# Kernel tuning notes

Measured on AMD Instinct MI355X. Metric: run time of the kernel, lower is better.

The kernel has to match this reference:

```python
import jax, jax.numpy as jnp
import numpy as np

NUM_EXPERTS = 8
HIDDEN = 2048
INTER = 4096
TOKENS = 8192  # divisible by NUM_EXPERTS


def setup_inputs() -> dict:
    key = jax.random.key(0)
    k1, k2, k3 = jax.random.split(key, 3)
    hidden_states = jax.random.normal(k1, (TOKENS, HIDDEN), dtype=jnp.float32)
    gate_up_proj = jax.random.normal(k2, (NUM_EXPERTS, HIDDEN, 2 * INTER), dtype=jnp.float32) * 0.02
    down_proj = jax.random.normal(k3, (NUM_EXPERTS, INTER, HIDDEN), dtype=jnp.float32) * 0.02
    return {"hidden_states": hidden_states, "gate_up_proj": gate_up_proj, "down_proj": down_proj}


def reference(hidden_states, gate_up_proj, down_proj):
    E, H = gate_up_proj.shape[0], gate_up_proj.shape[1]
    x = hidden_states.reshape(E, -1, H)                      # (E, T/E, H)
    gate_up = jnp.einsum('eth,ehf->etf', x, gate_up_proj)    # (E, T/E, 2I)
    gate, up = jnp.split(gate_up, 2, axis=-1)
    acted = up * jax.nn.silu(gate)                           # (E, T/E, I)
    out = jnp.einsum('eti,eih->eth', acted, down_proj)       # (E, T/E, H)
    return out.reshape(-1, H)
```

## Files before the change

kernel.cpp:

```cpp
#include <hip/hip_runtime.h>


#define E_   8
#define H_   2048
#define I_   4096
#define T_   8192
#define TPE  1024

typedef __bf16 bf16x8 __attribute__((ext_vector_type(8)));
typedef float  f32x4  __attribute__((ext_vector_type(4)));

__device__ __forceinline__ unsigned short f2bf(float f) {
  union { float f; unsigned int u; } v; v.f = f;
  unsigned int u = v.u;
  u += 0x7FFFu + ((u >> 16) & 1u);
  return (unsigned short)(u >> 16);
}

__device__ __forceinline__ void async16(const void* g, void* l) {
  __builtin_amdgcn_global_load_lds(
      (__attribute__((address_space(1))) void*)(g),
      (__attribute__((address_space(3))) void*)(l), 16, 0, 0);
}

#define SB0()    __builtin_amdgcn_sched_barrier(0)
#define BAR()    __builtin_amdgcn_s_barrier()
#define WAITLGKM() asm volatile("s_waitcnt lgkmcnt(0)" ::: "memory")
#define WAITVM(n)  asm volatile("s_waitcnt vmcnt(" #n ")" ::: "memory")

__global__ void convert_bf16(const float* __restrict__ src,
                             unsigned short* __restrict__ dst, long n) {
  long i = ((long)blockIdx.x * blockDim.x + threadIdx.x) * 4;
  const long stride = (long)gridDim.x * blockDim.x * 4;
  for (; i < n; i += stride) {
    const float4 v = *(const float4*)&src[i];
    ushort4 o;
    o.x = f2bf(v.x); o.y = f2bf(v.y); o.z = f2bf(v.z); o.w = f2bf(v.w);
    *(ushort4*)&dst[i] = o;
  }
}

template <int K, int NBN, int LDB, bool SILU>
__global__ __launch_bounds__(512, 2)
void gemm_fused(const unsigned short* __restrict__ Aall,
                const float* __restrict__ Ball,
                void* __restrict__ Cout,
                long sA, long sB, long sC) {
  extern __shared__ char smem[];
  constexpr int NT = K / 64;

  const int tid  = threadIdx.x;
  const int wave = tid >> 6;
  const int lane = tid & 63;
  const int lr   = lane & 15;
  const int lq   = lane >> 4;
  const int wid_m = wave >> 2;
  const int wid_n = wave & 3;

  const int nwg = gridDim.x;
  const int bid = blockIdx.x;
  const int wg  = (bid & 7) * (nwg >> 3) + (bid >> 3);
  const int mb  = wg & 3;
  const int tmp = wg >> 2;
  const int nb  = tmp % NBN;
  const int e   = tmp / NBN;

  const unsigned short* A = Aall + (long)e * sA + (long)(mb * 256) * K;
  const float*          B = Ball + (long)e * sB;

  const int stl  = tid >> 3;
  const int scol = ((tid & 7) ^ (stl & 7)) * 8;

  auto stageA = [&](int bi, int q, int kt) {
    const long col = (long)kt * 64 + scol;
    char* l0 = smem + bi * 32768 + q * 16384 + wave * 1024;
    async16(A + (long)(q * 64 + stl) * K + col,        l0);
    async16(A + (long)(128 + q * 64 + stl) * K + col,  l0 + 8192);
  };

  const int stB = tid & 255;
  int colg;
  {
    const int b  = stB >> 7;
    const int r  = stB & 127;
    const int w  = r >> 5;
    const int nf = (r >> 4) & 1;
    const int l4 = stB & 15;
    if (SILU) {
      const int c = w * 32 + b * 16 + l4;
      colg = nb * 128 + c + (nf ? I_ : 0);
    } else {
      colg = nb * 256 + w * 64 + (b * 2 + nf) * 16 + l4;
    }
  }
  const float* Bp = B + colg;
  const int koB = tid >> 8;

  float bv[16];
  auto loadB = [&](int g, int kt) {
#pragma unroll
    for (int uu = 0; uu < 2; ++uu) {
      const int ko = (g * 2 + uu) * 2 + koB;
      const long krow = (long)kt * 64 + ko * 8;
#pragma unroll
      for (int j = 0; j < 8; ++j)
        bv[uu * 8 + j] = Bp[(krow + j) * (long)LDB];
    }
  };
  auto writeB = [&](int bo, int g) {
    char* LB = smem + 65536 + bo * 32768;
#pragma unroll
    for (int uu = 0; uu < 2; ++uu) {
      const int ko = (g * 2 + uu) * 2 + koB;
      bf16x8 pk;
#pragma unroll
      for (int j = 0; j < 8; ++j) pk[j] = (__bf16)bv[uu * 8 + j];
      *(bf16x8*)(LB + stB * 128 + ((ko ^ (stB & 7)) * 16)) = pk;
    }
  };

  const int ax0 = ((0 + lq) ^ (lr & 7)) * 16;
  const int ax1 = ((4 + lq) ^ (lr & 7)) * 16;

  f32x4 acc[8][4];
#pragma unroll
  for (int m = 0; m < 8; ++m)
#pragma unroll
    for (int n = 0; n < 4; ++n) acc[m][n] = (f32x4)0.0f;

  const int t1p = (NT > 1) ? 1 : 0;
  loadB(0, 0);
  stageA(0, 0, 0);
  stageA(0, 1, 0);
  SB0();
  WAITVM(4);
  writeB(0, 0);
  loadB(1, 0);
  stageA(1, 0, t1p);
  stageA(1, 1, t1p);
  SB0();
  WAITVM(4);
  writeB(0, 1);
  WAITLGKM();
  BAR();

#pragma unroll 1
  for (int t = 0; t < NT; ++t) {
    const int cur = t & 1;
    const int bo  = cur ^ 1;
    const char* LA = smem + cur * 32768;
    const char* LB = smem + 65536 + cur * 32768;
    const int t1v = (t + 1 < NT) ? t + 1 : NT - 1;
    const int t2v = (t + 2 < NT) ? t + 2 : NT - 1;

    bf16x8 a[4][2], b0[2][2], b1[2][2];

#pragma unroll
    for (int mf = 0; mf < 4; ++mf) {
      const int st = wid_m * 64 + mf * 16 + lr;
      a[mf][0] = *(const bf16x8*)(LA + st * 128 + ax0);
      a[mf][1] = *(const bf16x8*)(LA + st * 128 + ax1);
    }
#pragma unroll
    for (int nf = 0; nf < 2; ++nf) {
      const int st = wid_n * 32 + nf * 16 + lr;
      b0[nf][0] = *(const bf16x8*)(LB + st * 128 + ax0);
      b0[nf][1] = *(const bf16x8*)(LB + st * 128 + ax1);
    }
    loadB(0, t1v);
    SB0();
    BAR();
    WAITLGKM();
    __builtin_amdgcn_s_setprio(1);
#pragma unroll
    for (int mf = 0; mf < 4; ++mf)
#pragma unroll
      for (int nf = 0; nf < 2; ++nf) {
        acc[mf][nf] = __builtin_amdgcn_mfma_f32_16x16x32_bf16(a[mf][0], b0[nf][0], acc[mf][nf], 0, 0, 0);
        acc[mf][nf] = __builtin_amdgcn_mfma_f32_16x16x32_bf16(a[mf][1], b0[nf][1], acc[mf][nf], 0, 0, 0);
      }
    __builtin_amdgcn_s_setprio(0);
    BAR();

#pragma unroll
    for (int nf = 0; nf < 2; ++nf) {
      const int st = 128 + wid_n * 32 + nf * 16 + lr;
      b1[nf][0] = *(const bf16x8*)(LB + st * 128 + ax0);
      b1[nf][1] = *(const bf16x8*)(LB + st * 128 + ax1);
    }
    stageA(cur, 0, t2v);
    SB0();
    BAR();
    WAITLGKM();
    __builtin_amdgcn_s_setprio(1);
#pragma unroll
    for (int mf = 0; mf < 4; ++mf)
#pragma unroll
      for (int nf = 0; nf < 2; ++nf) {
        acc[mf][2 + nf] = __builtin_amdgcn_mfma_f32_16x16x32_bf16(a[mf][0], b1[nf][0], acc[mf][2 + nf], 0, 0, 0);
        acc[mf][2 + nf] = __builtin_amdgcn_mfma_f32_16x16x32_bf16(a[mf][1], b1[nf][1], acc[mf][2 + nf], 0, 0, 0);
      }
    __builtin_amdgcn_s_setprio(0);
    BAR();

#pragma unroll
    for (int mf = 0; mf < 4; ++mf) {
      const int st = 128 + wid_m * 64 + mf * 16 + lr;
      a[mf][0] = *(const bf16x8*)(LA + st * 128 + ax0);
      a[mf][1] = *(const bf16x8*)(LA + st * 128 + ax1);
    }
    WAITVM(2);
    writeB(bo, 0);
    loadB(1, t1v);
    SB0();
    BAR();
    WAITLGKM();
    __builtin_amdgcn_s_setprio(1);
#pragma unroll
    for (int mf = 0; mf < 4; ++mf)
#pragma unroll
      for (int nf = 0; nf < 2; ++nf) {
        acc[4 + mf][2 + nf] = __builtin_amdgcn_mfma_f32_16x16x32_bf16(a[mf][0], b1[nf][0], acc[4 + mf][2 + nf], 0, 0, 0);
        acc[4 + mf][2 + nf] = __builtin_amdgcn_mfma_f32_16x16x32_bf16(a[mf][1], b1[nf][1], acc[4 + mf][2 + nf], 0, 0, 0);
      }
    __builtin_amdgcn_s_setprio(0);
    BAR();

    stageA(cur, 1, t2v);
    SB0();
    WAITVM(2);
    writeB(bo, 1);
    WAITLGKM();
    BAR();
    __builtin_amdgcn_s_setprio(1);
#pragma unroll
    for (int mf = 0; mf < 4; ++mf)
#pragma unroll
      for (int nf = 0; nf < 2; ++nf) {
        acc[4 + mf][nf] = __builtin_amdgcn_mfma_f32_16x16x32_bf16(a[mf][0], b0[nf][0], acc[4 + mf][nf], 0, 0, 0);
        acc[4 + mf][nf] = __builtin_amdgcn_mfma_f32_16x16x32_bf16(a[mf][1], b0[nf][1], acc[4 + mf][nf], 0, 0, 0);
      }
    __builtin_amdgcn_s_setprio(0);
    BAR();
  }

  const int lqq = lane >> 4;
  if (SILU) {
    unsigned short* Cc = (unsigned short*)Cout + (long)e * sC;
#pragma unroll
    for (int mf = 0; mf < 8; ++mf)
#pragma unroll
      for (int p = 0; p < 2; ++p)
#pragma unroll
        for (int rr = 0; rr < 4; ++rr) {
          const int row = mb * 256 + wid_m * 128 + mf * 16 + lqq * 4 + rr;
          const int col = nb * 128 + wid_n * 32 + p * 16 + lr;
          const float g = acc[mf][p * 2][rr];
          const float u = acc[mf][p * 2 + 1][rr];
          Cc[(long)row * I_ + col] = f2bf(u * (g / (1.0f + __expf(-g))));
        }
  } else {
    float* Cc = (float*)Cout + (long)e * sC;
#pragma unroll
    for (int mf = 0; mf < 8; ++mf)
#pragma unroll
      for (int q = 0; q < 4; ++q)
#pragma unroll
        for (int rr = 0; rr < 4; ++rr) {
          const int row = mb * 256 + wid_m * 128 + mf * 16 + lqq * 4 + rr;
          const int col = nb * 256 + wid_n * 64 + q * 16 + lr;
          Cc[(long)row * H_ + col] = acc[mf][q][rr];
        }
  }
}

extern "C" void kernel_launch(void* const* d_in, const int* in_sizes, int n_in,
                              void* d_out, int out_size, void* d_ws, size_t ws_size,
                              hipStream_t stream) {
  const float* hs = (const float*)d_in[0];
  const float* w1 = (const float*)d_in[1];
  const float* w2 = (const float*)d_in[2];
  float* out = (float*)d_out;
  char* ws = (char*)d_ws;

  const long HB_B  = (long)T_ * H_ * 2;
  const long ACT_B = (long)T_ * I_ * 2;
  if (ws_size < (size_t)(HB_B + ACT_B)) return;

  unsigned short* hiddenB = (unsigned short*)(ws);
  unsigned short* acted   = (unsigned short*)(ws + HB_B);

  hipLaunchKernelGGL(convert_bf16, dim3(2048), dim3(256), 0, stream,
                     hs, hiddenB, (long)T_ * H_);

  hipLaunchKernelGGL((gemm_fused<H_, 32, 2 * I_, true>),
                     dim3(1024), dim3(512), 131072, stream,
                     hiddenB, w1, acted,
                     (long)TPE * H_, (long)H_ * 2 * I_, (long)TPE * I_);

  hipLaunchKernelGGL((gemm_fused<I_, 8, H_, false>),
                     dim3(256), dim3(512), 131072, stream,
                     acted, w2, out,
                     (long)TPE * I_, (long)I_ * H_, (long)TPE * H_);
}
```

Baseline: 604.2 us.

## Prefetch B weights two tiles ahead using dual register buffers

Splits the B-weight register staging into two separate buffers, one per half of the k-tile, so global loads for tile t+2 are issued right after each half is written to LDS instead of loading tile t+1 at the start of the iteration. This deepens the prefetch distance for the strided fp32 weight loads to hide more of their latency behind MFMA work. In exchange it uses 16 more VGPRs for staging, which could pressure the 2-blocks-per-CU launch bound. The vmcnt wait thresholds and scheduling barriers are retuned to match the new ordering.

```diff
diff --git a/kernel.cpp b/kernel.cpp
--- a/kernel.cpp
+++ b/kernel.cpp
@@ -23,8 +23,8 @@
       (__attribute__((address_space(3))) void*)(l), 16, 0, 0);
 }
 
-#define SB0()    __builtin_amdgcn_sched_barrier(0)
-#define BAR()    __builtin_amdgcn_s_barrier()
+#define SB0()      __builtin_amdgcn_sched_barrier(0)
+#define BAR()      __builtin_amdgcn_s_barrier()
 #define WAITLGKM() asm volatile("s_waitcnt lgkmcnt(0)" ::: "memory")
 #define WAITVM(n)  asm volatile("s_waitcnt vmcnt(" #n ")" ::: "memory")
 
@@ -96,28 +96,31 @@
   const float* Bp = B + colg;
   const int koB = tid >> 8;
 
-  float bv[16];
-  auto loadB = [&](int g, int kt) {
-#pragma unroll
-    for (int uu = 0; uu < 2; ++uu) {
-      const int ko = (g * 2 + uu) * 2 + koB;
-      const long krow = (long)kt * 64 + ko * 8;
-#pragma unroll
-      for (int j = 0; j < 8; ++j)
-        bv[uu * 8 + j] = Bp[(krow + j) * (long)LDB];
-    }
-  };
-  auto writeB = [&](int bo, int g) {
-    char* LB = smem + 65536 + bo * 32768;
-#pragma unroll
-    for (int uu = 0; uu < 2; ++uu) {
-      const int ko = (g * 2 + uu) * 2 + koB;
-      bf16x8 pk;
-#pragma unroll
-      for (int j = 0; j < 8; ++j) pk[j] = (__bf16)bv[uu * 8 + j];
-      *(bf16x8*)(LB + stB * 128 + ((ko ^ (stB & 7)) * 16)) = pk;
-    }
-  };
+  float bvG1[16], bvG2[16];
+
+#define LOADB(BV, G, KT)                                                    \
+  do {                                                                      \
+    _Pragma("unroll")                                                       \
+    for (int uu = 0; uu < 2; ++uu) {                                        \
+      const int ko_ = ((G) * 2 + uu) * 2 + koB;                             \
+      const float* p_ = Bp + ((long)(KT) * 64 + ko_ * 8) * (long)LDB;       \
+      _Pragma("unroll")                                                     \
+      for (int j = 0; j < 8; ++j) BV[uu * 8 + j] = p_[j * (long)LDB];       \
+    }                                                                       \
+  } while (0)
+
+#define WRITEB(BO, BV, G)                                                   \
+  do {                                                                      \
+    char* LBw_ = smem + 65536 + (BO) * 32768;                               \
+    _Pragma("unroll")                                                       \
+    for (int uu = 0; uu < 2; ++uu) {                                        \
+      const int ko_ = ((G) * 2 + uu) * 2 + koB;                             \
+      bf16x8 pk_;                                                           \
+      _Pragma("unroll")                                                     \
+      for (int j = 0; j < 8; ++j) pk_[j] = (__bf16)BV[uu * 8 + j];          \
+      *(bf16x8*)(LBw_ + stB * 128 + ((ko_ ^ (stB & 7)) * 16)) = pk_;        \
+    }                                                                       \
+  } while (0)
 
   const int ax0 = ((0 + lq) ^ (lr & 7)) * 16;
   const int ax1 = ((4 + lq) ^ (lr & 7)) * 16;
@@ -129,19 +132,21 @@
     for (int n = 0; n < 4; ++n) acc[m][n] = (f32x4)0.0f;
 
   const int t1p = (NT > 1) ? 1 : 0;
-  loadB(0, 0);
+  LOADB(bvG1, 0, 0);
+  LOADB(bvG2, 1, 0);
   stageA(0, 0, 0);
   stageA(0, 1, 0);
   SB0();
-  WAITVM(4);
-  writeB(0, 0);
-  loadB(1, 0);
-  stageA(1, 0, t1p);
-  stageA(1, 1, t1p);
-  SB0();
-  WAITVM(4);
-  writeB(0, 1);
-  WAITLGKM();
+  WAITVM(20); SB0();
+  WRITEB(0, bvG1, 0);
+  WAITVM(4); SB0();
+  WRITEB(0, bvG2, 1);
+  WAITLGKM(); SB0();
+  stageA(1, 0, t1p); SB0();
+  LOADB(bvG1, 0, t1p); SB0();
+  stageA(1, 1, t1p); SB0();
+  LOADB(bvG2, 1, t1p); SB0();
+  WAITVM(36); SB0();
   BAR();
 
 #pragma unroll 1
@@ -150,7 +155,6 @@
     const int bo  = cur ^ 1;
     const char* LA = smem + cur * 32768;
     const char* LB = smem + 65536 + cur * 32768;
-    const int t1v = (t + 1 < NT) ? t + 1 : NT - 1;
     const int t2v = (t + 2 < NT) ? t + 2 : NT - 1;
 
     bf16x8 a[4][2], b0[2][2], b1[2][2];
@@ -167,10 +171,9 @@
       b0[nf][0] = *(const bf16x8*)(LB + st * 128 + ax0);
       b0[nf][1] = *(const bf16x8*)(LB + st * 128 + ax1);
     }
-    loadB(0, t1v);
-    SB0();
-    BAR();
-    WAITLGKM();
+    SB0();
+    BAR();
+    WAITLGKM(); SB0();
     __builtin_amdgcn_s_setprio(1);
 #pragma unroll
     for (int mf = 0; mf < 4; ++mf)
@@ -191,7 +194,7 @@
     stageA(cur, 0, t2v);
     SB0();
     BAR();
-    WAITLGKM();
+    WAITLGKM(); SB0();
     __builtin_amdgcn_s_setprio(1);
 #pragma unroll
     for (int mf = 0; mf < 4; ++mf)
@@ -209,12 +212,13 @@
       a[mf][0] = *(const bf16x8*)(LA + st * 128 + ax0);
       a[mf][1] = *(const bf16x8*)(LA + st * 128 + ax1);
     }
-    WAITVM(2);
-    writeB(bo, 0);
-    loadB(1, t1v);
-    SB0();
-    BAR();
-    WAITLGKM();
+    SB0();
+    WAITVM(20); SB0();
+    WRITEB(bo, bvG1, 0);
+    WAITLGKM(); SB0();
+    LOADB(bvG1, 0, t2v);
+    SB0();
+    BAR();
     __builtin_amdgcn_s_setprio(1);
 #pragma unroll
     for (int mf = 0; mf < 4; ++mf)
@@ -228,9 +232,11 @@
 
     stageA(cur, 1, t2v);
     SB0();
-    WAITVM(2);
-    writeB(bo, 1);
-    WAITLGKM();
+    WAITVM(20); SB0();
+    WRITEB(bo, bvG2, 1);
+    WAITLGKM(); SB0();
+    LOADB(bvG2, 1, t2v);
+    SB0();
     BAR();
     __builtin_amdgcn_s_setprio(1);
 #pragma unroll
@@ -244,7 +250,6 @@
     BAR();
   }
 
-  const int lqq = lane >> 4;
   if (SILU) {
     unsigned short* Cc = (unsigned short*)Cout + (long)e * sC;
 #pragma unroll
@@ -253,7 +258,7 @@
       for (int p = 0; p < 2; ++p)
 #pragma unroll
         for (int rr = 0; rr < 4; ++rr) {
-          const int row = mb * 256 + wid_m * 128 + mf * 16 + lqq * 4 + rr;
+          const int row = mb * 256 + wid_m * 128 + mf * 16 + lq * 4 + rr;
           const int col = nb * 128 + wid_n * 32 + p * 16 + lr;
           const float g = acc[mf][p * 2][rr];
           const float u = acc[mf][p * 2 + 1][rr];
@@ -267,11 +272,13 @@
       for (int q = 0; q < 4; ++q)
 #pragma unroll
         for (int rr = 0; rr < 4; ++rr) {
-          const int row = mb * 256 + wid_m * 128 + mf * 16 + lqq * 4 + rr;
+          const int row = mb * 256 + wid_m * 128 + mf * 16 + lq * 4 + rr;
           const int col = nb * 256 + wid_n * 64 + q * 16 + lr;
           Cc[(long)row * H_ + col] = acc[mf][q][rr];
         }
   }
+#undef LOADB
+#undef WRITEB
 }
 
 extern "C" void kernel_launch(void* const* d_in, const int* in_sizes, int n_in,
```

Result: faster. 585.3 us (-3.1%).
